# Optimization experiments

Hardware: AMD Instinct MI355X
Metric: run time of the kernel (lower is better)

## Reference

```python
import jax, jax.numpy as jnp
import numpy as np

B, T, D_IN, D_OUT = 4, 2048, 1024, 1024


def setup_inputs() -> dict:
    key = jax.random.key(0)
    k1, k2, k3, k4 = jax.random.split(key, 4)
    s_in = 1.0 / np.sqrt(D_IN)
    return {
        "input_vector": jax.random.normal(k1, (B, T, D_IN), dtype=jnp.float32),
        "w_q": jax.random.normal(k2, (D_IN, D_OUT), dtype=jnp.float32) * s_in,
        "w_k": jax.random.normal(k3, (D_IN, D_OUT), dtype=jnp.float32) * s_in,
        "w_v": jax.random.normal(k4, (D_IN, D_OUT), dtype=jnp.float32) * s_in,
    }


def reference(input_vector, w_q, w_k, w_v):
    # projections: [B, T, D_OUT]
    q = jnp.einsum("btd,de->bte", input_vector, w_q)
    k = jnp.einsum("btd,de->bte", input_vector, w_k)
    v = jnp.einsum("btd,de->bte", input_vector, w_v)

    T_ = q.shape[1]
    # raw scores [B, T, T]
    scores = jnp.einsum("bqd,bkd->bqk", q, k)
    # causal mask (strict upper triangle masked to -inf), applied BEFORE scaling
    # (as in the original; -inf is invariant under the scale anyway)
    causal = jnp.tril(jnp.ones((T_, T_), dtype=bool))  # True = keep
    scores = jnp.where(causal[None, :, :], scores, -jnp.inf)
    scores = scores / jnp.sqrt(jnp.asarray(k.shape[-1], scores.dtype))
    attn = jax.nn.softmax(scores, axis=-1)
    # dropout = 0.0 (eval): identity
    return jnp.einsum("bqk,bkd->bqd", attn, v)
```

## Files before the change

kernel.cpp:

```cpp
#include <hip/hip_runtime.h>
#include <cstdint>
#include <math.h>

typedef unsigned short u16;
typedef __attribute__((ext_vector_type(8))) short short8;
typedef __attribute__((ext_vector_type(4))) float f32x4;

__device__ __forceinline__ u16 f2bf(float f) {
  uint32_t u = __float_as_uint(f);
  u += 0x7FFFu + ((u >> 16) & 1u);
  return (u16)(u >> 16);
}
__device__ __forceinline__ float bf2f(u16 h) {
  return __uint_as_float(((uint32_t)h) << 16);
}

__device__ __forceinline__ void async_ld16(u16* lds, const u16* g) {
  __builtin_amdgcn_global_load_lds((const __attribute__((address_space(1))) uint32_t*)g,
                                   (__attribute__((address_space(3))) uint32_t*)lds,
                                   16, 0, 0);
}

template <bool OUT_BF16, int MODE, bool KLIM>
__global__ __launch_bounds__(256) void gemm_bt(
    const u16* __restrict__ A, int lda, long zsA,
    const u16* __restrict__ B, int ldb, long zsB,
    void* __restrict__ Cv, int ldc, long zsC,
    int K, float scale, int NB)
{
  const int b = blockIdx.x, zb = blockIdx.y;
  int nb, mb;
  if constexpr (MODE == 1) {
    const int u = b & 7, v = b >> 3;
    nb = v & (NB - 1);
    mb = u * ((int)(gridDim.x >> 3) / NB) + (v / NB);
  } else if constexpr (MODE == 2) {
    const int u = b & 7, idx = b >> 3;
    if (idx <= u) { mb = u;      nb = idx; }
    else          { mb = 15 - u; nb = idx - u - 1; }
  } else if constexpr (MODE == 3) {
    const int u = b & 7, idx = b >> 3;
    mb = (idx < 8) ? u : 15 - u;
    nb = idx & 7;
  } else {
    nb = b % NB;
    mb = b / NB;
  }

  A += (long)zb * zsA;
  B += (long)zb * zsB;
  const int m0 = mb * 128, n0 = nb * 128;

  __shared__ __align__(16) u16 lsA[128 * 32];
  __shared__ __align__(16) u16 lsB[128 * 32];

  const int tid = threadIdx.x;
  const int lane = tid & 63;
  const int wave = tid >> 6;
  const int wr = (wave >> 1) * 64;
  const int wc = (wave & 1) * 64;

  f32x4 acc[4][4];
#pragma unroll
  for (int i = 0; i < 4; ++i)
#pragma unroll
    for (int j = 0; j < 4; ++j) acc[i][j] = (f32x4){0.f, 0.f, 0.f, 0.f};

  const int c0 = tid;
  const int c1 = tid + 256;
  const int r0 = c0 >> 2, q0 = (c0 & 3) * 8;
  const int r1 = c1 >> 2, q1 = (c1 & 3) * 8;

  const int fm = lane & 15;
  const int fq = (lane >> 4) * 8;

  const int klim = (mb + 1) * 128;
  const int kmax = KLIM ? (K < klim ? K : klim) : K;

  const long gA0 = (long)(m0 + r0) * lda + q0;
  const long gA1 = (long)(m0 + r1) * lda + q1;
  const long gB0 = (long)(n0 + r0) * ldb + q0;
  const long gB1 = (long)(n0 + r1) * ldb + q1;

  for (int k0 = 0; k0 < kmax; k0 += 32) {
    __syncthreads();
    async_ld16(&lsA[c0 * 8], A + gA0 + k0);
    async_ld16(&lsA[c1 * 8], A + gA1 + k0);
    async_ld16(&lsB[c0 * 8], B + gB0 + k0);
    async_ld16(&lsB[c1 * 8], B + gB1 + k0);
    __syncthreads();

    short8 af[4], bfr[4];
#pragma unroll
    for (int i = 0; i < 4; ++i)
      af[i] = *(const short8*)&lsA[(wr + i * 16 + fm) * 32 + fq];
#pragma unroll
    for (int j = 0; j < 4; ++j)
      bfr[j] = *(const short8*)&lsB[(wc + j * 16 + fm) * 32 + fq];

#pragma unroll
    for (int i = 0; i < 4; ++i)
#pragma unroll
      for (int j = 0; j < 4; ++j)
        acc[i][j] = __builtin_amdgcn_mfma_f32_16x16x32_bf16(af[i], bfr[j], acc[i][j], 0, 0, 0);
  }

  const int er = (lane >> 4) * 4;
  const int ec = lane & 15;

  if constexpr (OUT_BF16) {
    u16* C = (u16*)Cv + (long)zb * zsC;
#pragma unroll
    for (int i = 0; i < 4; ++i) {
      const int row = m0 + wr + i * 16 + er;
#pragma unroll
      for (int j = 0; j < 4; ++j) {
        const int col = n0 + wc + j * 16 + ec;
#pragma unroll
        for (int r = 0; r < 4; ++r)
          C[(long)(row + r) * ldc + col] = f2bf(acc[i][j][r] * scale);
      }
    }
  } else {
    float* C = (float*)Cv + (long)zb * zsC;
#pragma unroll
    for (int i = 0; i < 4; ++i) {
      const int row = m0 + wr + i * 16 + er;
#pragma unroll
      for (int j = 0; j < 4; ++j) {
        const int col = n0 + wc + j * 16 + ec;
#pragma unroll
        for (int r = 0; r < 4; ++r)
          C[(long)(row + r) * ldc + col] = acc[i][j][r] * scale;
      }
    }
  }
}

__global__ __launch_bounds__(256) void cast_x_kernel(const float* __restrict__ x,
                                                     u16* __restrict__ y) {
  const long i = ((long)blockIdx.x * 256 + threadIdx.x) * 4;
  const float4 v = *(const float4*)(x + i);
  ushort4 o;
  o.x = f2bf(v.x); o.y = f2bf(v.y); o.z = f2bf(v.z); o.w = f2bf(v.w);
  *(ushort4*)(y + i) = o;
}

__global__ __launch_bounds__(256) void cast_wt_kernel(const float* __restrict__ w0,
                                                      const float* __restrict__ w1,
                                                      const float* __restrict__ w2,
                                                      u16* __restrict__ Wt) {
  const float* W = (blockIdx.z == 0) ? w0 : (blockIdx.z == 1) ? w1 : w2;
  u16* o = Wt + (long)blockIdx.z * 1024 * 1024;
  __shared__ float t[32][33];
  const int n0 = blockIdx.x * 32, k0 = blockIdx.y * 32;
  const int tx = threadIdx.x, ty = threadIdx.y;
  for (int r = ty; r < 32; r += 8) t[r][tx] = W[(long)(k0 + r) * 1024 + n0 + tx];
  __syncthreads();
  for (int r = ty; r < 32; r += 8) o[(long)(n0 + r) * 1024 + k0 + tx] = f2bf(t[tx][r]);
}

__global__ __launch_bounds__(256) void transpose_v_kernel(const u16* __restrict__ V,
                                                          u16* __restrict__ Vt) {
  __shared__ u16 t[32][33];
  const int d0 = blockIdx.x * 32, t0 = blockIdx.y * 32, b = blockIdx.z;
  const u16* Vb = V + (long)b * 2048 * 1024;
  u16* Ob = Vt + (long)b * 1024 * 2048;
  const int tx = threadIdx.x, ty = threadIdx.y;
  for (int r = ty; r < 32; r += 8) t[r][tx] = Vb[(long)(t0 + r) * 1024 + d0 + tx];
  __syncthreads();
  for (int r = ty; r < 32; r += 8) Ob[(long)(d0 + r) * 2048 + t0 + tx] = t[tx][r];
}

__global__ __launch_bounds__(256) void softmax_rows(const u16* __restrict__ S,
                                                    u16* __restrict__ P, int T) {
  const int q = blockIdx.x, b = blockIdx.y;
  const u16* srow = S + ((long)b * T + q) * T;
  u16* prow = P + ((long)b * T + q) * T;
  const int L = q + 1;
  const int Lpad = ((q >> 7) + 1) << 7;
  const int tid = threadIdx.x;

  float sv[8];
  float m = -3.4e38f;
#pragma unroll
  for (int i = 0; i < 8; ++i) {
    const int j = tid + i * 256;
    sv[i] = (j < L) ? bf2f(srow[j]) : -3.4e38f;
    m = fmaxf(m, sv[i]);
  }
#pragma unroll
  for (int off = 32; off > 0; off >>= 1) m = fmaxf(m, __shfl_down(m, off, 64));

  __shared__ float red[4];
  __shared__ float bcast;
  if ((tid & 63) == 0) red[tid >> 6] = m;
  __syncthreads();
  if (tid == 0) bcast = fmaxf(fmaxf(red[0], red[1]), fmaxf(red[2], red[3]));
  __syncthreads();
  m = bcast;

  float s = 0.f;
#pragma unroll
  for (int i = 0; i < 8; ++i) {
    const int j = tid + i * 256;
    sv[i] = (j < L) ? __expf(sv[i] - m) : 0.f;
    s += sv[i];
  }
#pragma unroll
  for (int off = 32; off > 0; off >>= 1) s += __shfl_down(s, off, 64);
  __syncthreads();
  if ((tid & 63) == 0) red[tid >> 6] = s;
  __syncthreads();
  if (tid == 0) bcast = red[0] + red[1] + red[2] + red[3];
  __syncthreads();
  const float inv = 1.f / bcast;

#pragma unroll
  for (int i = 0; i < 8; ++i) {
    const int j = tid + i * 256;
    if (j < Lpad) prow[j] = f2bf(sv[i] * inv);
  }
}

extern "C" void kernel_launch(void* const* d_in, const int* in_sizes, int n_in,
                              void* d_out, int out_size, void* d_ws, size_t ws_size,
                              hipStream_t stream) {
  const float* X  = (const float*)d_in[0];
  const float* Wq = (const float*)d_in[1];
  const float* Wk = (const float*)d_in[2];
  const float* Wv = (const float*)d_in[3];
  float* out = (float*)d_out;

  const long BT = 8192;
  const long Tq = 2048, D = 1024;

  u16* Xbf = (u16*)d_ws;
  u16* Wt  = Xbf + BT * D;
  u16* QKV = Wt + 3 * D * D;
  u16* Vt  = QKV + 3 * BT * D;
  u16* Sb  = Vt + 4 * D * Tq;
  u16* P   = Sb + 4 * Tq * Tq;

  cast_x_kernel<<<8192, 256, 0, stream>>>(X, Xbf);
  cast_wt_kernel<<<dim3(32, 32, 3), dim3(32, 8), 0, stream>>>(Wq, Wk, Wv, Wt);

  gemm_bt<true, 1, false><<<dim3(512, 3), 256, 0, stream>>>(
      Xbf, 1024, 0L, Wt, 1024, D * D, QKV, 1024, BT * D, 1024, 1.0f, 8);

  gemm_bt<true, 2, false><<<dim3(136, 4), 256, 0, stream>>>(
      QKV, 1024, Tq * D, QKV + BT * D, 1024, Tq * D,
      Sb, 2048, Tq * Tq, 1024, 0.03125f, 16);

  softmax_rows<<<dim3(2048, 4), 256, 0, stream>>>(Sb, P, 2048);

  transpose_v_kernel<<<dim3(32, 64, 4), dim3(32, 8), 0, stream>>>(QKV + 2 * BT * D, Vt);

  gemm_bt<false, 3, true><<<dim3(128, 4), 256, 0, stream>>>(
      P, 2048, Tq * Tq, Vt, 2048, D * Tq,
      out, 1024, Tq * D, 2048, 1.0f, 8);
}
```

Before: 282.8 us.

## Switch GEMM to 32x32x16 MFMA with XOR-swizzled LDS layout

Replaces the 16x16x32 bf16 MFMA tiling (4x4 fragments per wave) with 32x32x16 MFMA (2x2 fragments, two k-steps per 32-wide tile). This cuts the number of LDS fragment reads and MFMA issues per k-step. The global-to-LDS load column chunks are now XOR-swizzled by row to avoid LDS bank conflicts, and the reads use matching swizzled offsets. The epilogue is rewritten for the 32x32 accumulator row/column mapping.

```diff
diff --git a/kernel.cpp b/kernel.cpp
--- a/kernel.cpp
+++ b/kernel.cpp
@@ -4,7 +4,7 @@
 
 typedef unsigned short u16;
 typedef __attribute__((ext_vector_type(8))) short short8;
-typedef __attribute__((ext_vector_type(4))) float f32x4;
+typedef __attribute__((ext_vector_type(16))) float f32x16;
 
 __device__ __forceinline__ u16 f2bf(float f) {
   uint32_t u = __float_as_uint(f);
@@ -60,78 +60,93 @@
   const int wr = (wave >> 1) * 64;
   const int wc = (wave & 1) * 64;
 
-  f32x4 acc[4][4];
-#pragma unroll
-  for (int i = 0; i < 4; ++i)
-#pragma unroll
-    for (int j = 0; j < 4; ++j) acc[i][j] = (f32x4){0.f, 0.f, 0.f, 0.f};
+  f32x16 acc[2][2];
+#pragma unroll
+  for (int i = 0; i < 2; ++i)
+#pragma unroll
+    for (int j = 0; j < 2; ++j)
+#pragma unroll
+      for (int r = 0; r < 16; ++r) acc[i][j][r] = 0.f;
 
   const int c0 = tid;
   const int c1 = tid + 256;
-  const int r0 = c0 >> 2, q0 = (c0 & 3) * 8;
-  const int r1 = c1 >> 2, q1 = (c1 & 3) * 8;
-
-  const int fm = lane & 15;
-  const int fq = (lane >> 4) * 8;
+  const int r0 = c0 >> 2, q0 = (((c0 & 3) ^ (r0 & 3))) * 8;
+  const int r1 = c1 >> 2, q1 = (((c1 & 3) ^ (r1 & 3))) * 8;
 
   const int klim = (mb + 1) * 128;
   const int kmax = KLIM ? (K < klim ? K : klim) : K;
 
-  const long gA0 = (long)(m0 + r0) * lda + q0;
-  const long gA1 = (long)(m0 + r1) * lda + q1;
-  const long gB0 = (long)(n0 + r0) * ldb + q0;
-  const long gB1 = (long)(n0 + r1) * ldb + q1;
+  const u16* pA0 = A + (long)(m0 + r0) * lda + q0;
+  const u16* pA1 = A + (long)(m0 + r1) * lda + q1;
+  const u16* pB0 = B + (long)(n0 + r0) * ldb + q0;
+  const u16* pB1 = B + (long)(n0 + r1) * ldb + q1;
+
+  const int m32 = lane & 31;
+  const int hh = lane >> 5;
+  const int sw = lane & 3;
+  int offA[2][2], offB[2][2];
+#pragma unroll
+  for (int i = 0; i < 2; ++i)
+#pragma unroll
+    for (int ks = 0; ks < 2; ++ks) {
+      const int kq = ((ks << 1) | hh) ^ sw;
+      offA[i][ks] = (wr + i * 32 + m32) * 32 + kq * 8;
+      offB[i][ks] = (wc + i * 32 + m32) * 32 + kq * 8;
+    }
 
   for (int k0 = 0; k0 < kmax; k0 += 32) {
     __syncthreads();
-    async_ld16(&lsA[c0 * 8], A + gA0 + k0);
-    async_ld16(&lsA[c1 * 8], A + gA1 + k0);
-    async_ld16(&lsB[c0 * 8], B + gB0 + k0);
-    async_ld16(&lsB[c1 * 8], B + gB1 + k0);
+    async_ld16(&lsA[c0 * 8], pA0);
+    async_ld16(&lsA[c1 * 8], pA1);
+    async_ld16(&lsB[c0 * 8], pB0);
+    async_ld16(&lsB[c1 * 8], pB1);
+    pA0 += 32; pA1 += 32; pB0 += 32; pB1 += 32;
     __syncthreads();
 
-    short8 af[4], bfr[4];
-#pragma unroll
-    for (int i = 0; i < 4; ++i)
-      af[i] = *(const short8*)&lsA[(wr + i * 16 + fm) * 32 + fq];
-#pragma unroll
-    for (int j = 0; j < 4; ++j)
-      bfr[j] = *(const short8*)&lsB[(wc + j * 16 + fm) * 32 + fq];
-
-#pragma unroll
-    for (int i = 0; i < 4; ++i)
-#pragma unroll
-      for (int j = 0; j < 4; ++j)
-        acc[i][j] = __builtin_amdgcn_mfma_f32_16x16x32_bf16(af[i], bfr[j], acc[i][j], 0, 0, 0);
-  }
-
-  const int er = (lane >> 4) * 4;
-  const int ec = lane & 15;
+#pragma unroll
+    for (int ks = 0; ks < 2; ++ks) {
+      const short8 a0 = *(const short8*)&lsA[offA[0][ks]];
+      const short8 a1 = *(const short8*)&lsA[offA[1][ks]];
+      const short8 b0 = *(const short8*)&lsB[offB[0][ks]];
+      const short8 b1 = *(const short8*)&lsB[offB[1][ks]];
+      acc[0][0] = __builtin_amdgcn_mfma_f32_32x32x16_bf16(a0, b0, acc[0][0], 0, 0, 0);
+      acc[0][1] = __builtin_amdgcn_mfma_f32_32x32x16_bf16(a0, b1, acc[0][1], 0, 0, 0);
+      acc[1][0] = __builtin_amdgcn_mfma_f32_32x32x16_bf16(a1, b0, acc[1][0], 0, 0, 0);
+      acc[1][1] = __builtin_amdgcn_mfma_f32_32x32x16_bf16(a1, b1, acc[1][1], 0, 0, 0);
+    }
+  }
+
+  const int ec = lane & 31;
+  const int rb = (lane >> 5) * 4;
 
   if constexpr (OUT_BF16) {
     u16* C = (u16*)Cv + (long)zb * zsC;
 #pragma unroll
-    for (int i = 0; i < 4; ++i) {
-      const int row = m0 + wr + i * 16 + er;
-#pragma unroll
-      for (int j = 0; j < 4; ++j) {
-        const int col = n0 + wc + j * 16 + ec;
-#pragma unroll
-        for (int r = 0; r < 4; ++r)
-          C[(long)(row + r) * ldc + col] = f2bf(acc[i][j][r] * scale);
+    for (int i = 0; i < 2; ++i) {
+      const int rbase = m0 + wr + i * 32 + rb;
+#pragma unroll
+      for (int j = 0; j < 2; ++j) {
+        const int col = n0 + wc + j * 32 + ec;
+#pragma unroll
+        for (int r = 0; r < 16; ++r) {
+          const int row = rbase + (r & 3) + 8 * (r >> 2);
+          C[(long)row * ldc + col] = f2bf(acc[i][j][r] * scale);
+        }
       }
     }
   } else {
     float* C = (float*)Cv + (long)zb * zsC;
 #pragma unroll
-    for (int i = 0; i < 4; ++i) {
-      const int row = m0 + wr + i * 16 + er;
-#pragma unroll
-      for (int j = 0; j < 4; ++j) {
-        const int col = n0 + wc + j * 16 + ec;
-#pragma unroll
-        for (int r = 0; r < 4; ++r)
-          C[(long)(row + r) * ldc + col] = acc[i][j][r] * scale;
+    for (int i = 0; i < 2; ++i) {
+      const int rbase = m0 + wr + i * 32 + rb;
+#pragma unroll
+      for (int j = 0; j < 2; ++j) {
+        const int col = n0 + wc + j * 32 + ec;
+#pragma unroll
+        for (int r = 0; r < 16; ++r) {
+          const int row = rbase + (r & 3) + 8 * (r >> 2);
+          C[(long)row * ldc + col] = acc[i][j][r] * scale;
+        }
       }
     }
   }
```

New measurement: 280.6 us. About the same (-0.8%).
